# Optimization experiments

Measured on AMD Instinct MI355X. Metric: run time of the kernel, lower is better.

Reference implementation:

```python
import jax, jax.numpy as jnp
import numpy as np

B, G, T, N = 4, 8, 30, 60
CT, CN = 1, 60
FD, IDD = 256, 256
E = FD + IDD          # 512
H = 8                 # (FD+IDD)//head_dim
L = 6                 # num_layers
VP1 = 51              # num_id_vocabulary + 1
PE = 32               # rel_pe_length
DFF = 4 * E


def _ln(x, g, b, eps=1e-5):
    m = x.mean(-1, keepdims=True)
    v = ((x - m) ** 2).mean(-1, keepdims=True)
    return (x - m) / jnp.sqrt(v + eps) * g + b


def _mha(qx, kx, vx, Wqkv, bqkv, Wo, bo, bias, h):
    # torch nn.MultiheadAttention with add_zero_attn=True; bias is additive
    # attn bias of shape [B, h, Lq, Lk+1] (already padded for the zero-attn col).
    e = qx.shape[-1]
    d = e // h
    Wq, Wk, Wv = jnp.split(Wqkv, 3, axis=0)
    bq, bk, bv = jnp.split(bqkv, 3)
    q = qx @ Wq.T + bq
    k = kx @ Wk.T + bk
    v = vx @ Wv.T + bv
    b_, lq, _ = q.shape
    lk = k.shape[1]
    z = jnp.zeros((b_, 1, e), q.dtype)
    k = jnp.concatenate([k, z], axis=1)   # add_zero_attn appends zero key
    v = jnp.concatenate([v, z], axis=1)
    qh = q.reshape(b_, lq, h, d).transpose(0, 2, 1, 3)
    kh = k.reshape(b_, lk + 1, h, d).transpose(0, 2, 1, 3)
    vh = v.reshape(b_, lk + 1, h, d).transpose(0, 2, 1, 3)
    s = jnp.einsum('bhqd,bhkd->bhqk', qh, kh) / jnp.sqrt(jnp.float32(d)) + bias
    p = jax.nn.softmax(s, axis=-1)
    o = jnp.einsum('bhqk,bhkd->bhqd', p, vh).transpose(0, 2, 1, 3).reshape(b_, lq, e)
    return o @ Wo.T + bo


def _forward(tf, uf, ids, tt_, ut_, tm, um, Ww, Wout, rpe,
             saW, sab, saO, saob, sag, sabn,
             caW, cab, caO, caob, cag, cabn,
             f1, fb1, f2, fb2, fg, fbn):
    b, g, t, n, fd = tf.shape
    _, _, ct, cn, _ = uf.shape
    id_dim = Ww.shape[0]
    e = fd + id_dim
    nl = caW.shape[0]
    h = rpe.shape[-1]
    pe = rpe.shape[1]
    # one_hot(label) @ W_word.T == W_word[:, label]
    traj_id = Ww.T[ids]                                        # b g t n id
    unk_id = jnp.broadcast_to(Ww[:, VP1 - 1], (b, g, ct, cn, id_dim))
    traj = jnp.concatenate([tf, traj_id], -1).reshape(b * g, t * n, e)
    unk = jnp.concatenate([uf, unk_id], -1)                    # b g ct cn e

    tt = tt_.reshape(b * g, t * n)
    ut = ut_.reshape(b * g, ct * cn)
    neg = jnp.float32(-jnp.inf)
    zero = jnp.float32(0)
    causal = jnp.where(tt[:, None, :] >= ut[:, :, None], neg, zero)  # bg q k
    kpm = jnp.where(tm.reshape(b * g, t * n), neg, zero)             # bg k
    # torch rel_pos_map[u, t] = u - t; negative torch indices wrap -> mod pe
    rel_idx = (ut[:, :, None] - tt[:, None, :]) % pe                 # bg q k
    sa_bias = jnp.pad(
        jnp.where(um.reshape(b * g * ct, cn), neg, zero)[:, None, None, :],
        ((0, 0), (0, 0), (0, 0), (0, 1)))

    for l in range(nl):
        if l > 0:
            x = unk.reshape(b * g * ct, cn, e)
            y = _mha(x, x, x, saW[l - 1], sab[l - 1], saO[l - 1], saob[l - 1], sa_bias, h)
            unk = _ln(x + y, sag[l - 1], sabn[l - 1]).reshape(b, g, ct, cn, e)
        q = unk.reshape(b * g, ct * cn, e)
        rel = rpe[l][rel_idx]                                  # bg q k h  (gathered rel-PE)
        bias = causal[:, None] + jnp.transpose(rel, (0, 3, 1, 2)) + kpm[:, None, None, :]
        bias = jnp.pad(bias, ((0, 0), (0, 0), (0, 0), (0, 1)))
        y = _mha(q, traj, traj, caW[l], cab[l], caO[l], caob[l], bias, h)
        x = _ln(q + y, cag[l], cabn[l])
        hh = jax.nn.gelu(x @ f1[l].T + fb1[l], approximate=False) @ f2[l].T + fb2[l]
        x = _ln(x + hh, fg[l], fbn[l])
        unk = x.reshape(b, g, ct, cn, e)
    # final layer logits (eval mode): shared embed_to_word head, no bias
    return unk[..., fd:] @ Wout.T


def setup_inputs():
    key = jax.random.key(0)
    ks = iter(jax.random.split(key, 48))
    nrm = lambda shape, s=0.02: jax.random.normal(next(ks), shape, jnp.float32) * s
    return {
        'trajectory_features': jax.random.normal(next(ks), (B, G, T, N, FD), jnp.float32),
        'unknown_features': jax.random.normal(next(ks), (B, G, CT, CN, FD), jnp.float32),
        'trajectory_id_labels': jax.random.randint(next(ks), (B, G, T, N), 0, VP1),
        'trajectory_times': jax.random.randint(next(ks), (B, G, T, N), 0, PE),
        'unknown_times': jax.random.randint(next(ks), (B, G, CT, CN), 0, PE),
        'trajectory_masks': jnp.zeros((B, G, T, N), bool),
        'unknown_masks': jnp.zeros((B, G, CT, CN), bool),
        'use_decoder_checkpoint': 0,
        'W_word': nrm((IDD, VP1), 0.05),
        'W_out': nrm((VP1, IDD), 0.05),
        'rel_pos_embeds': nrm((L, PE, H), 0.1),
        'sa_Wqkv': nrm((L - 1, 3 * E, E)), 'sa_bqkv': jnp.zeros((L - 1, 3 * E)),
        'sa_Wo': nrm((L - 1, E, E)), 'sa_bo': jnp.zeros((L - 1, E)),
        'sa_ln_g': jnp.ones((L - 1, E)), 'sa_ln_b': jnp.zeros((L - 1, E)),
        'ca_Wqkv': nrm((L, 3 * E, E)), 'ca_bqkv': jnp.zeros((L, 3 * E)),
        'ca_Wo': nrm((L, E, E)), 'ca_bo': jnp.zeros((L, E)),
        'ca_ln_g': jnp.ones((L, E)), 'ca_ln_b': jnp.zeros((L, E)),
        'ffn_W1': nrm((L, DFF, E)), 'ffn_b1': jnp.zeros((L, DFF)),
        'ffn_W2': nrm((L, E, DFF)), 'ffn_b2': jnp.zeros((L, E)),
        'ffn_ln_g': jnp.ones((L, E)), 'ffn_ln_b': jnp.zeros((L, E)),
    }


def reference(trajectory_features, unknown_features, trajectory_id_labels,
              trajectory_times, unknown_times, trajectory_masks, unknown_masks,
              use_decoder_checkpoint, W_word, W_out, rel_pos_embeds,
              sa_Wqkv, sa_bqkv, sa_Wo, sa_bo, sa_ln_g, sa_ln_b,
              ca_Wqkv, ca_bqkv, ca_Wo, ca_bo, ca_ln_g, ca_ln_b,
              ffn_W1, ffn_b1, ffn_W2, ffn_b2, ffn_ln_g, ffn_ln_b):
    return _forward(trajectory_features, unknown_features, trajectory_id_labels,
                    trajectory_times, unknown_times, trajectory_masks, unknown_masks,
                    W_word, W_out, rel_pos_embeds,
                    sa_Wqkv, sa_bqkv, sa_Wo, sa_bo, sa_ln_g, sa_ln_b,
                    ca_Wqkv, ca_bqkv, ca_Wo, ca_bo, ca_ln_g, ca_ln_b,
                    ffn_W1, ffn_b1, ffn_W2, ffn_b2, ffn_ln_g, ffn_ln_b)
```

## Files before the change

kernel.cpp:

```cpp
#include <hip/hip_runtime.h>
#include <cmath>

__device__ __forceinline__ float bflo(unsigned int u) {
  union { unsigned int i; float f; } v; v.i = u << 16; return v.f;
}
__device__ __forceinline__ float bfhi(unsigned int u) {
  union { unsigned int i; float f; } v; v.i = u & 0xffff0000u; return v.f;
}
__device__ __forceinline__ float bf2f(unsigned short u) {
  union { unsigned int i; float f; } v; v.i = ((unsigned int)u) << 16; return v.f;
}
__device__ __forceinline__ unsigned short f2bf(float f) {
  union { float f; unsigned int i; } v; v.f = f;
  unsigned int i = v.i;
  return (unsigned short)((i + 0x7fffu + ((i >> 16) & 1u)) >> 16);
}

typedef __attribute__((ext_vector_type(8))) short short8;
typedef __attribute__((ext_vector_type(4))) float floatx4;

__global__ __launch_bounds__(256) void conv_kernel(
    const float* __restrict__ in, unsigned short* __restrict__ out, int n)
{
  int i = (blockIdx.x * 256 + threadIdx.x) << 2;
  if (i >= n) return;
  float4 v = *reinterpret_cast<const float4*>(in + i);
  ushort4 o;
  o.x = f2bf(v.x); o.y = f2bf(v.y); o.z = f2bf(v.z); o.w = f2bf(v.w);
  *reinterpret_cast<ushort4*>(out + i) = o;
}

__global__ __launch_bounds__(256) void gemm_mfma(
    const unsigned short* __restrict__ A, int lda,
    const unsigned short* __restrict__ W, int ldw,
    const float* __restrict__ bias,
    void* __restrict__ Cv, int ldc,
    int K, int act, int cbf16, int swz)
{
  __shared__ __align__(16) unsigned short As[2][128 * 32];
  __shared__ __align__(16) unsigned short Bs[2][128 * 32];
  const int tid = threadIdx.x;
  const int wave = tid >> 6, lane = tid & 63;

  int bxi = blockIdx.x, byi = blockIdx.y;
  if (swz) {
    int f = byi * gridDim.x + bxi;
    int q = (gridDim.x * gridDim.y) >> 3;
    f = (f & 7) * q + (f >> 3);
    bxi = f % gridDim.x;
    byi = f / gridDim.x;
  }
  const int bm = byi * 128, bn = bxi * 128;
  const int wm = (wave >> 1) << 6, wn = (wave & 1) << 6;

  floatx4 acc[4][4];
#pragma unroll
  for (int i = 0; i < 4; ++i)
#pragma unroll
    for (int j = 0; j < 4; ++j) acc[i][j] = (floatx4){0.f, 0.f, 0.f, 0.f};

  const int srow = (wave << 5) + (lane >> 2);
  const int chsw = (lane & 3) ^ ((srow >> 1) & 3);
  const int scol = chsw << 3;
  const unsigned short* Ag  = A + (size_t)(bm + srow) * lda + scol;
  const unsigned short* Wg  = W + (size_t)(bn + srow) * ldw + scol;
  const unsigned short* Ag2 = Ag + (size_t)16 * lda;
  const unsigned short* Wg2 = Wg + (size_t)16 * ldw;
  const int ldsw = (wave << 5) * 32;

  const int arow = lane & 15;
  const int rsw  = (arow >> 1) & 3;
  const int chrd = (lane >> 4) ^ rsw;
  const int aoff = (wm + arow) * 32 + (chrd << 3);
  const int boff = (wn + arow) * 32 + (chrd << 3);

  const int nt = K >> 5;

#define STAGE(b, t)                                                                 \
  do {                                                                              \
    const int k0_ = (t) << 5;                                                       \
    __builtin_amdgcn_global_load_lds(                                               \
        (const __attribute__((address_space(1))) unsigned int*)(Ag + k0_),          \
        (__attribute__((address_space(3))) unsigned int*)(As[(b)] + ldsw), 16, 0, 0); \
    __builtin_amdgcn_global_load_lds(                                               \
        (const __attribute__((address_space(1))) unsigned int*)(Ag2 + k0_),         \
        (__attribute__((address_space(3))) unsigned int*)(As[(b)] + ldsw + 16 * 32), 16, 0, 0); \
    __builtin_amdgcn_global_load_lds(                                               \
        (const __attribute__((address_space(1))) unsigned int*)(Wg + k0_),          \
        (__attribute__((address_space(3))) unsigned int*)(Bs[(b)] + ldsw), 16, 0, 0); \
    __builtin_amdgcn_global_load_lds(                                               \
        (const __attribute__((address_space(1))) unsigned int*)(Wg2 + k0_),         \
        (__attribute__((address_space(3))) unsigned int*)(Bs[(b)] + ldsw + 16 * 32), 16, 0, 0); \
  } while (0)

  STAGE(0, 0);
  if (nt > 1) STAGE(1, 1);

  int cur = 0;
  for (int t = 0; t < nt; ++t) {
    if (t + 1 < nt) asm volatile("s_waitcnt vmcnt(4)\n\ts_barrier" ::: "memory");
    else            asm volatile("s_waitcnt vmcnt(0)\n\ts_barrier" ::: "memory");

    short8 af[4], bf[4];
#pragma unroll
    for (int i = 0; i < 4; ++i) {
      af[i] = *reinterpret_cast<const short8*>(&As[cur][aoff + (i << 4) * 32]);
      bf[i] = *reinterpret_cast<const short8*>(&Bs[cur][boff + (i << 4) * 32]);
    }
    asm volatile("s_waitcnt lgkmcnt(0)\n\ts_barrier" ::: "memory");
    if (t + 2 < nt) STAGE(cur, t + 2);

#pragma unroll
    for (int i = 0; i < 4; ++i)
#pragma unroll
      for (int j = 0; j < 4; ++j)
        acc[i][j] = __builtin_amdgcn_mfma_f32_16x16x32_bf16(af[i], bf[j], acc[i][j], 0, 0, 0);
    cur ^= 1;
  }
#undef STAGE

  const int col0 = lane & 15;
  const int row0 = (lane >> 4) << 2;
#pragma unroll
  for (int i = 0; i < 4; ++i) {
#pragma unroll
    for (int j = 0; j < 4; ++j) {
      int col = bn + wn + (j << 4) + col0;
      float bv = bias ? bias[col] : 0.f;
#pragma unroll
      for (int r = 0; r < 4; ++r) {
        int row = bm + wm + (i << 4) + row0 + r;
        float v = acc[i][j][r] + bv;
        if (act) v = 0.5f * v * (1.f + erff(v * 0.70710678f));
        if (cbf16) ((unsigned short*)Cv)[(size_t)row * ldc + col] = f2bf(v);
        else       ((float*)Cv)[(size_t)row * ldc + col] = v;
      }
    }
  }
}

__device__ __forceinline__ float wred_max(float v) {
#pragma unroll
  for (int off = 32; off > 0; off >>= 1) v = fmaxf(v, __shfl_xor(v, off, 64));
  return v;
}
__device__ __forceinline__ float wred_sum(float v) {
#pragma unroll
  for (int off = 32; off > 0; off >>= 1) v += __shfl_xor(v, off, 64);
  return v;
}

#define LDK 72
__global__ __launch_bounds__(512) void attn_mfma_kernel(
    const unsigned short* __restrict__ Qp,
    const unsigned short* __restrict__ KVb,
    unsigned short* __restrict__ O,
    const int* __restrict__ tt, const int* __restrict__ ut,
    const unsigned char* __restrict__ km,
    const float* __restrict__ rel)
{
  const int bg = blockIdx.x >> 3, h = blockIdx.x & 7;
  const int tid = threadIdx.x;
  const int grp = tid >> 8;
  const int wave = (tid >> 6) & 3;
  const int lane = tid & 63;
  const int quad = lane >> 4, mrow = lane & 15;

  __shared__ __align__(16) unsigned short SMEM[6 * 64 * LDK];
  unsigned short* Ks = SMEM + grp * (3 * 64 * LDK);
  unsigned short* Vt = Ks + 64 * LDK;
  unsigned short* Ps = Vt + 64 * LDK;

  const int qa = wave * 16 + mrow;
  const int qc = qa < 60 ? qa : 59;
  const unsigned short* qptr = Qp + (size_t)(bg * 60 + qc) * 512 + h * 64 + quad * 8;
  const short8 af0 = *reinterpret_cast<const short8*>(qptr);
  const short8 af1 = *reinterpret_cast<const short8*>(qptr + 32);

  const float relreg = rel[(lane & 31) * 8 + h];

  int tq[4];
  float m[4], l[4];
  floatx4 acc[4];
#pragma unroll
  for (int r = 0; r < 4; ++r) {
    int qo = wave * 16 + quad * 4 + r;
    tq[r] = ut[bg * 60 + (qo < 60 ? qo : 59)];
    m[r] = grp ? -1e30f : 0.f;
    l[r] = grp ? 0.f : 1.f;
  }
#pragma unroll
  for (int nt = 0; nt < 4; ++nt) acc[nt] = (floatx4){0.f, 0.f, 0.f, 0.f};

  const int sk = tid & 255;
  const int stok = sk >> 2, schk = sk & 3;

  for (int it = 0; it < 15; ++it) {
    const int k0 = (grp + 2 * it) << 6;
    __syncthreads();
    {
      const int key = k0 + stok;
      uint4 kr0 = {0,0,0,0}, kr1 = {0,0,0,0}, vr0 = {0,0,0,0}, vr1 = {0,0,0,0};
      if (key < 1800) {
        const unsigned short* kb = KVb + ((size_t)bg * 1800 + key) * 1024 + h * 64 + schk * 16;
        kr0 = *reinterpret_cast<const uint4*>(kb);
        kr1 = *reinterpret_cast<const uint4*>(kb + 8);
        vr0 = *reinterpret_cast<const uint4*>(kb + 512);
        vr1 = *reinterpret_cast<const uint4*>(kb + 520);
      }
      *reinterpret_cast<uint4*>(&Ks[stok * LDK + schk * 16]) = kr0;
      *reinterpret_cast<uint4*>(&Ks[stok * LDK + schk * 16 + 8]) = kr1;
      unsigned int wv[8] = {vr0.x, vr0.y, vr0.z, vr0.w, vr1.x, vr1.y, vr1.z, vr1.w};
#pragma unroll
      for (int e = 0; e < 16; ++e)
        Vt[(schk * 16 + e) * LDK + stok] = (unsigned short)(wv[e >> 1] >> ((e & 1) * 16));
    }
    int meta = 0x10000;
    {
      int kk = k0 + lane;
      if (kk < 1800) {
        int base = bg * 1800 + kk;
        meta = tt[base] | (km[base] ? 0x10000 : 0);
      }
    }
    __syncthreads();

    floatx4 S[4];
#pragma unroll
    for (int nt = 0; nt < 4; ++nt) {
      const unsigned short* kb = Ks + (nt * 16 + mrow) * LDK + quad * 8;
      short8 b0 = *reinterpret_cast<const short8*>(kb);
      short8 b1 = *reinterpret_cast<const short8*>(kb + 32);
      floatx4 s = (floatx4){0.f, 0.f, 0.f, 0.f};
      s = __builtin_amdgcn_mfma_f32_16x16x32_bf16(af0, b0, s, 0, 0, 0);
      s = __builtin_amdgcn_mfma_f32_16x16x32_bf16(af1, b1, s, 0, 0, 0);
      S[nt] = s;
    }
    int mcol[4];
#pragma unroll
    for (int nt = 0; nt < 4; ++nt)
      mcol[nt] = __builtin_amdgcn_ds_bpermute((nt * 16 + mrow) << 2, meta);
    float sv[4][4];
#pragma unroll
    for (int nt = 0; nt < 4; ++nt) {
      int tk = mcol[nt] & 0xffff;
      int bad0 = mcol[nt] >> 16;
#pragma unroll
      for (int r = 0; r < 4; ++r) {
        float v = S[nt][r] * 0.125f;
        int ridx = (tq[r] - tk) & 31;
        v += __int_as_float(__builtin_amdgcn_ds_bpermute(ridx << 2, __float_as_int(relreg)));
        sv[nt][r] = (bad0 | (tk >= tq[r])) ? -1e30f : v;
      }
    }
#pragma unroll
    for (int r = 0; r < 4; ++r) {
      float rm = fmaxf(fmaxf(sv[0][r], sv[1][r]), fmaxf(sv[2][r], sv[3][r]));
#pragma unroll
      for (int d = 1; d < 16; d <<= 1) rm = fmaxf(rm, __shfl_xor(rm, d, 64));
      float nm = fmaxf(m[r], rm);
      float corr = __expf(m[r] - nm);
      float ps = 0.f;
      const int prow = (wave * 16 + quad * 4 + r) * LDK + mrow;
#pragma unroll
      for (int nt = 0; nt < 4; ++nt) {
        float p = __expf(sv[nt][r] - nm);
        ps += p;
        Ps[prow + nt * 16] = f2bf(p);
      }
#pragma unroll
      for (int d = 1; d < 16; d <<= 1) ps += __shfl_xor(ps, d, 64);
      l[r] = l[r] * corr + ps;
      m[r] = nm;
#pragma unroll
      for (int nt = 0; nt < 4; ++nt) acc[nt][r] *= corr;
    }
    const unsigned short* pp = Ps + (wave * 16 + mrow) * LDK + quad * 8;
    short8 a0 = *reinterpret_cast<const short8*>(pp);
    short8 a1 = *reinterpret_cast<const short8*>(pp + 32);
#pragma unroll
    for (int nt = 0; nt < 4; ++nt) {
      const unsigned short* vb = Vt + (nt * 16 + mrow) * LDK + quad * 8;
      short8 b0 = *reinterpret_cast<const short8*>(vb);
      short8 b1 = *reinterpret_cast<const short8*>(vb + 32);
      acc[nt] = __builtin_amdgcn_mfma_f32_16x16x32_bf16(a0, b0, acc[nt], 0, 0, 0);
      acc[nt] = __builtin_amdgcn_mfma_f32_16x16x32_bf16(a1, b1, acc[nt], 0, 0, 0);
    }
  }

  __syncthreads();
  float* MA = (float*)SMEM;
  float* Ml = (float*)(SMEM + 64 * 68 * 2);
  float* Ll = Ml + 64;
  if (grp == 1) {
#pragma unroll
    for (int r = 0; r < 4; ++r) {
      int row = wave * 16 + quad * 4 + r;
#pragma unroll
      for (int nt = 0; nt < 4; ++nt)
        MA[row * 68 + nt * 16 + mrow] = acc[nt][r];
      if (mrow == 0) { Ml[row] = m[r]; Ll[row] = l[r]; }
    }
  }
  __syncthreads();
  if (grp == 0) {
#pragma unroll
    for (int r = 0; r < 4; ++r) {
      int row = wave * 16 + quad * 4 + r;
      float m1 = Ml[row], l1 = Ll[row];
      float M = fmaxf(m[r], m1);
      float c0 = __expf(m[r] - M), c1 = __expf(m1 - M);
      float invL = 1.f / (l[r] * c0 + l1 * c1);
      if (row < 60) {
        unsigned short* op = O + (size_t)(bg * 60 + row) * 512 + h * 64;
#pragma unroll
        for (int nt = 0; nt < 4; ++nt) {
          float o = (acc[nt][r] * c0 + MA[row * 68 + nt * 16 + mrow] * c1) * invL;
          op[nt * 16 + mrow] = f2bf(o);
        }
      }
    }
  }
}

#define QPB 32
#define QPW 8
__global__ __launch_bounds__(256) void attn2_kernel(
    const unsigned short* __restrict__ Qp, int qs,
    const unsigned short* __restrict__ Kp, int ks,
    const unsigned short* __restrict__ Vp, int vs,
    unsigned short* __restrict__ O, int os, int kLen,
    const unsigned char* __restrict__ kmask)
{
  const int bg = blockIdx.x >> 3;
  const int h  = blockIdx.x & 7;
  const int q0 = blockIdx.y * QPB;
  const int tid = threadIdx.x;
  const int wave = tid >> 6, lane = tid & 63;

  __shared__ float Qs[QPB][68];
  __shared__ float Ks[64][68];
  __shared__ float Vs[64][68];
  __shared__ float Ps[QPB][68];

  {
    int qr = tid >> 3, j = tid & 7;
    int q = q0 + qr;
    float f[8] = {0, 0, 0, 0, 0, 0, 0, 0};
    if (q < 60) {
      uint4 v = *reinterpret_cast<const uint4*>(Qp + (size_t)(bg * 60 + q) * qs + h * 64 + j * 8);
      f[0] = bflo(v.x); f[1] = bfhi(v.x); f[2] = bflo(v.y); f[3] = bfhi(v.y);
      f[4] = bflo(v.z); f[5] = bfhi(v.z); f[6] = bflo(v.w); f[7] = bfhi(v.w);
    }
#pragma unroll
    for (int e = 0; e < 8; ++e) Qs[qr][j * 8 + e] = f[e];
  }

  float m[QPW], l[QPW], acc[QPW];
#pragma unroll
  for (int i = 0; i < QPW; ++i) { m[i] = 0.f; l[i] = 1.f; acc[i] = 0.f; }

  const int std = tid >> 2;
  const int stj = tid & 3;

  for (int k0 = 0; k0 < kLen; k0 += 64) {
    __syncthreads();
    const bool sok = (k0 + std) < kLen;
    {
      const unsigned short* kb = Kp + ((size_t)bg * kLen + k0 + std) * ks + h * 64 + stj * 16;
      float f[16];
#pragma unroll
      for (int e = 0; e < 16; ++e) f[e] = 0.f;
      if (sok) {
        uint4 v0 = *reinterpret_cast<const uint4*>(kb);
        uint4 v1 = *reinterpret_cast<const uint4*>(kb + 8);
        f[0] = bflo(v0.x); f[1] = bfhi(v0.x); f[2]  = bflo(v0.y); f[3]  = bfhi(v0.y);
        f[4] = bflo(v0.z); f[5] = bfhi(v0.z); f[6]  = bflo(v0.w); f[7]  = bfhi(v0.w);
        f[8] = bflo(v1.x); f[9] = bfhi(v1.x); f[10] = bflo(v1.y); f[11] = bfhi(v1.y);
        f[12] = bflo(v1.z); f[13] = bfhi(v1.z); f[14] = bflo(v1.w); f[15] = bfhi(v1.w);
      }
#pragma unroll
      for (int e = 0; e < 16; ++e) Ks[stj * 16 + e][std] = f[e];
    }
    {
      const unsigned short* vb = Vp + ((size_t)bg * kLen + k0 + std) * vs + h * 64;
#pragma unroll
      for (int c = 0; c < 2; ++c) {
        int off = c * 32 + stj * 8;
        float f[8] = {0, 0, 0, 0, 0, 0, 0, 0};
        if (sok) {
          uint4 v = *reinterpret_cast<const uint4*>(vb + off);
          f[0] = bflo(v.x); f[1] = bfhi(v.x); f[2] = bflo(v.y); f[3] = bfhi(v.y);
          f[4] = bflo(v.z); f[5] = bfhi(v.z); f[6] = bflo(v.w); f[7] = bfhi(v.w);
        }
#pragma unroll
        for (int e = 0; e < 8; ++e) Vs[std][off + e] = f[e];
      }
    }
    const int kk = k0 + lane;
    const bool kok = kk < kLen;
    unsigned char kmv = 0;
    if (kok && kmask) kmv = kmask[(size_t)bg * kLen + kk];
    __syncthreads();

    float s[QPW];
#pragma unroll
    for (int i = 0; i < QPW; ++i) s[i] = 0.f;
    for (int d = 0; d < 64; ++d) {
      float kv = Ks[d][lane];
#pragma unroll
      for (int i = 0; i < QPW; ++i)
        s[i] = fmaf(Qs[wave * QPW + i][d], kv, s[i]);
    }

    const int kmax = min(64, kLen - k0);
#pragma unroll
    for (int i = 0; i < QPW; ++i) {
      float svv = s[i] * 0.125f;
      if (kmv || !kok) svv = -1e30f;
      float nm = fmaxf(m[i], wred_max(svv));
      float p = __expf(svv - nm);
      float ts = wred_sum(p);
      float corr = __expf(m[i] - nm);
      l[i] = l[i] * corr + ts;
      acc[i] *= corr;
      m[i] = nm;
      Ps[wave * QPW + i][lane] = p;
    }
    for (int k = 0; k < kmax; ++k) {
      float v = Vs[k][lane];
#pragma unroll
      for (int i = 0; i < QPW; ++i)
        acc[i] = fmaf(Ps[wave * QPW + i][k], v, acc[i]);
    }
  }

#pragma unroll
  for (int i = 0; i < QPW; ++i) {
    int q = q0 + wave * QPW + i;
    if (q < 60)
      O[(size_t)(bg * 60 + q) * os + h * 64 + lane] = f2bf(acc[i] / l[i]);
  }
}

__global__ __launch_bounds__(256) void add_ln_kernel(
    const float* __restrict__ a, const float* __restrict__ b,
    const float* __restrict__ g, const float* __restrict__ be,
    float* __restrict__ o, unsigned short* __restrict__ ob)
{
  const int t = blockIdx.x;
  const int tid = threadIdx.x;
  const int wave = tid >> 6, lane = tid & 63;
  const size_t base = (size_t)t * 512;
  float v0 = a[base + tid] + b[base + tid];
  float v1 = a[base + 256 + tid] + b[base + 256 + tid];
  __shared__ float red[4];
  float s = wred_sum(v0 + v1);
  if (lane == 0) red[wave] = s;
  __syncthreads();
  float mean = (red[0] + red[1] + red[2] + red[3]) * (1.0f / 512.0f);
  float d0 = v0 - mean, d1 = v1 - mean;
  float vs = wred_sum(d0 * d0 + d1 * d1);
  __syncthreads();
  if (lane == 0) red[wave] = vs;
  __syncthreads();
  float var = (red[0] + red[1] + red[2] + red[3]) * (1.0f / 512.0f);
  float rstd = rsqrtf(var + 1e-5f);
  float r0 = d0 * rstd * g[tid] + be[tid];
  float r1 = d1 * rstd * g[256 + tid] + be[256 + tid];
  o[base + tid] = r0;
  o[base + 256 + tid] = r1;
  ob[base + tid] = f2bf(r0);
  ob[base + 256 + tid] = f2bf(r1);
}

__global__ __launch_bounds__(256) void build_traj_kernel(
    const float* __restrict__ tf, const int* __restrict__ ids,
    const float* __restrict__ Ww, unsigned short* __restrict__ traj)
{
  int idx = blockIdx.x * 256 + threadIdx.x;
  int tok = idx >> 9;
  int j = idx & 511;
  float v = (j < 256) ? tf[((size_t)tok << 8) + j] : Ww[(j - 256) * 51 + ids[tok]];
  traj[idx] = f2bf(v);
}

__global__ __launch_bounds__(256) void build_unk_kernel(
    const float* __restrict__ uf, const float* __restrict__ Ww,
    float* __restrict__ x, unsigned short* __restrict__ xb)
{
  int idx = blockIdx.x * 256 + threadIdx.x;
  int tok = idx >> 9;
  int j = idx & 511;
  float v = (j < 256) ? uf[((size_t)tok << 8) + j] : Ww[(j - 256) * 51 + 50];
  x[idx] = v;
  xb[idx] = f2bf(v);
}

__global__ __launch_bounds__(64) void head_kernel(
    const float* __restrict__ x, const float* __restrict__ Wout, float* __restrict__ out)
{
  const int t = blockIdx.x;
  const int tid = threadIdx.x;
  __shared__ float xs[256];
  for (int i = tid; i < 256; i += 64) xs[i] = x[(size_t)t * 512 + 256 + i];
  __syncthreads();
  if (tid < 51) {
    const float* w = Wout + tid * 256;
    float s = 0.f;
    for (int k = 0; k < 256; ++k) s = fmaf(xs[k], w[k], s);
    out[t * 51 + tid] = s;
  }
}

extern "C" void kernel_launch(void* const* d_in, const int* in_sizes, int n_in,
                              void* d_out, int out_size, void* d_ws, size_t ws_size,
                              hipStream_t stream) {
  const float* tf  = (const float*)d_in[0];
  const float* uf  = (const float*)d_in[1];
  const int*   ids = (const int*)d_in[2];
  const int*   tt  = (const int*)d_in[3];
  const int*   ut  = (const int*)d_in[4];
  const unsigned char* tm = (const unsigned char*)d_in[5];
  const unsigned char* um = (const unsigned char*)d_in[6];
  const float* Ww   = (const float*)d_in[8];
  const float* Wout = (const float*)d_in[9];
  const float* rpe  = (const float*)d_in[10];
  const float* saW  = (const float*)d_in[11];
  const float* sab  = (const float*)d_in[12];
  const float* saO  = (const float*)d_in[13];
  const float* saob = (const float*)d_in[14];
  const float* sag  = (const float*)d_in[15];
  const float* sabn = (const float*)d_in[16];
  const float* caW  = (const float*)d_in[17];
  const float* cab  = (const float*)d_in[18];
  const float* caO  = (const float*)d_in[19];
  const float* caob = (const float*)d_in[20];
  const float* cag  = (const float*)d_in[21];
  const float* cabn = (const float*)d_in[22];
  const float* f1   = (const float*)d_in[23];
  const float* fb1  = (const float*)d_in[24];
  const float* f2   = (const float*)d_in[25];
  const float* fb2  = (const float*)d_in[26];
  const float* fg   = (const float*)d_in[27];
  const float* fbn  = (const float*)d_in[28];

  unsigned short* trajb = (unsigned short*)d_ws;
  unsigned short* KVb   = trajb + (size_t)29491200;
  unsigned short* qkvb  = KVb   + (size_t)58982400;
  unsigned short* hb    = qkvb  + (size_t)2949120;
  unsigned short* xb    = hb    + (size_t)3932160;
  float* x    = (float*)(xb + (size_t)983040);
  float* ybuf = x + (size_t)983040;
  unsigned short* wtail = (unsigned short*)(ybuf + (size_t)983040);

  const size_t NEED = (size_t)200540160 + (size_t)24117248 * 2;
  const bool pre = ws_size >= NEED;
  unsigned short* wsa  = wtail;
  unsigned short* wsaO = wsa  + (size_t)3932160;
  unsigned short* wca  = wsaO + (size_t)1310720;
  unsigned short* wcaO = wca  + (size_t)4718592;
  unsigned short* wf1  = wcaO + (size_t)1572864;
  unsigned short* wf2  = wf1  + (size_t)6291456;
  unsigned short* wconv = wtail;

  if (pre) {
    conv_kernel<<<dim3(3840), dim3(256), 0, stream>>>(saW, wsa, 3932160);
    conv_kernel<<<dim3(1280), dim3(256), 0, stream>>>(saO, wsaO, 1310720);
    conv_kernel<<<dim3(4608), dim3(256), 0, stream>>>(caW, wca, 4718592);
    conv_kernel<<<dim3(1536), dim3(256), 0, stream>>>(caO, wcaO, 1572864);
    conv_kernel<<<dim3(6144), dim3(256), 0, stream>>>(f1, wf1, 6291456);
    conv_kernel<<<dim3(6144), dim3(256), 0, stream>>>(f2, wf2, 6291456);
  }

  build_traj_kernel<<<dim3(115200), dim3(256), 0, stream>>>(tf, ids, Ww, trajb);
  build_unk_kernel<<<dim3(3840), dim3(256), 0, stream>>>(uf, Ww, x, xb);

  for (int l = 0; l < 6; ++l) {
    if (l > 0) {
      int sl = l - 1;
      const unsigned short* wq;
      if (pre) wq = wsa + (size_t)sl * 786432;
      else {
        conv_kernel<<<dim3(768), dim3(256), 0, stream>>>(saW + (size_t)sl * 786432, wconv, 786432);
        wq = wconv;
      }
      gemm_mfma<<<dim3(12, 15), dim3(256), 0, stream>>>(
          xb, 512, wq, 512, sab + sl * 1536, qkvb, 1536, 512, 0, 1, 0);
      attn2_kernel<<<dim3(256, 2), dim3(256), 0, stream>>>(
          qkvb, 1536, qkvb + 512, 1536, qkvb + 1024, 1536, hb, 512, 60, um);
      const unsigned short* wo;
      if (pre) wo = wsaO + (size_t)sl * 262144;
      else {
        conv_kernel<<<dim3(256), dim3(256), 0, stream>>>(saO + (size_t)sl * 262144, wconv, 262144);
        wo = wconv;
      }
      gemm_mfma<<<dim3(4, 15), dim3(256), 0, stream>>>(
          hb, 512, wo, 512, saob + sl * 512, ybuf, 512, 512, 0, 0, 0);
      add_ln_kernel<<<dim3(1920), dim3(256), 0, stream>>>(x, ybuf, sag + sl * 512, sabn + sl * 512, x, xb);
    }
    const unsigned short* wqkv;
    if (pre) wqkv = wca + (size_t)l * 786432;
    else {
      conv_kernel<<<dim3(768), dim3(256), 0, stream>>>(caW + (size_t)l * 786432, wconv, 786432);
      wqkv = wconv;
    }
    gemm_mfma<<<dim3(8, 450), dim3(256), 0, stream>>>(
        trajb, 512, wqkv + 262144, 512, cab + l * 1536 + 512, KVb, 1024, 512, 0, 1, 1);
    gemm_mfma<<<dim3(4, 15), dim3(256), 0, stream>>>(
        xb, 512, wqkv, 512, cab + l * 1536, qkvb, 512, 512, 0, 1, 0);
    attn_mfma_kernel<<<dim3(256), dim3(512), 0, stream>>>(
        qkvb, KVb, hb, tt, ut, tm, rpe + l * 256);
    const unsigned short* wco;
    if (pre) wco = wcaO + (size_t)l * 262144;
    else {
      conv_kernel<<<dim3(256), dim3(256), 0, stream>>>(caO + (size_t)l * 262144, wconv, 262144);
      wco = wconv;
    }
    gemm_mfma<<<dim3(4, 15), dim3(256), 0, stream>>>(
        hb, 512, wco, 512, caob + l * 512, ybuf, 512, 512, 0, 0, 0);
    add_ln_kernel<<<dim3(1920), dim3(256), 0, stream>>>(x, ybuf, cag + l * 512, cabn + l * 512, x, xb);
    const unsigned short* w1;
    if (pre) w1 = wf1 + (size_t)l * 1048576;
    else {
      conv_kernel<<<dim3(1024), dim3(256), 0, stream>>>(f1 + (size_t)l * 1048576, wconv, 1048576);
      w1 = wconv;
    }
    gemm_mfma<<<dim3(16, 15), dim3(256), 0, stream>>>(
        xb, 512, w1, 512, fb1 + l * 2048, hb, 2048, 512, 1, 1, 0);
    const unsigned short* w2;
    if (pre) w2 = wf2 + (size_t)l * 1048576;
    else {
      conv_kernel<<<dim3(1024), dim3(256), 0, stream>>>(f2 + (size_t)l * 1048576, wconv, 1048576);
      w2 = wconv;
    }
    gemm_mfma<<<dim3(4, 15), dim3(256), 0, stream>>>(
        hb, 2048, w2, 2048, fb2 + l * 512, ybuf, 512, 2048, 0, 0, 0);
    add_ln_kernel<<<dim3(1920), dim3(256), 0, stream>>>(x, ybuf, fg + l * 512, fbn + l * 512, x, xb);
  }
  head_kernel<<<dim3(1920), dim3(64), 0, stream>>>(x, Wout, (float*)d_out);
}
```

Measured before the change: 1.995 ms.

## Add 256x256-tile GEMM with direct-to-LDS loads for cross-attention KV projection

Adds a dedicated 256x256 tile GEMM kernel for the large cross-attention K/V projection (57600x1024x512). It uses 512 threads, double-buffered LDS filled by global_load_lds, swizzled LDS reads, fine-grained staging interleaved with MFMA blocks, s_setprio and an XCD-aware block remap. The aim is more operand reuse per tile and better overlap of loads with compute than the generic 128x128 gemm_mfma. In exchange it hardcodes K=512, N=1024 and M divisible by 256, and its large register footprint may limit occupancy.

```diff
diff --git a/kernel.cpp b/kernel.cpp
--- a/kernel.cpp
+++ b/kernel.cpp
@@ -28,6 +28,165 @@
   ushort4 o;
   o.x = f2bf(v.x); o.y = f2bf(v.y); o.z = f2bf(v.z); o.w = f2bf(v.w);
   *reinterpret_cast<ushort4*>(out + i) = o;
+}
+
+__global__ __launch_bounds__(512, 2) void gemm256(
+    const unsigned short* __restrict__ A,
+    const unsigned short* __restrict__ W,
+    const float* __restrict__ bias,
+    unsigned short* __restrict__ C)
+{
+  __shared__ __align__(16) unsigned short LA[2][2][8192];
+  __shared__ __align__(16) unsigned short LB[2][2][8192];
+  const int tid = threadIdx.x;
+  const int wave = tid >> 6, lane = tid & 63;
+  const int quad = lane >> 4, mrow = lane & 15;
+  const int wm = wave >> 2, wn = wave & 3;
+  const size_t ldK = 512;
+  const int nt = 8;
+
+  int f = blockIdx.x;
+  {
+    const int nwg = gridDim.x;
+    const int q = nwg >> 3, r = nwg & 7;
+    const int x = f & 7, i = f >> 3;
+    f = (x < r ? x * (q + 1) : r * (q + 1) + (x - r) * q) + i;
+  }
+  const int bn = (f & 3) << 8;
+  const int bm = (f >> 2) << 8;
+
+  floatx4 acc[8][4];
+#pragma unroll
+  for (int i = 0; i < 8; ++i)
+#pragma unroll
+    for (int j = 0; j < 4; ++j) acc[i][j] = (floatx4){0.f, 0.f, 0.f, 0.f};
+
+  const int srow0 = (wave << 4) + (lane >> 2);
+  const int srow1 = srow0 + 128;
+  const int sslot = (lane & 3) ^ (srow0 & 3);
+
+#define STAGEH(dst, srcbase, rowoff, kelem)                                          \
+  do {                                                                               \
+    __builtin_amdgcn_global_load_lds(                                                \
+        (const __attribute__((address_space(1))) unsigned int*)(                     \
+            (srcbase) + (size_t)((rowoff) + srow0) * ldK + (kelem) + sslot * 8),     \
+        (__attribute__((address_space(3))) unsigned int*)((dst) + wave * 512),       \
+        16, 0, 0);                                                                   \
+    __builtin_amdgcn_global_load_lds(                                                \
+        (const __attribute__((address_space(1))) unsigned int*)(                     \
+            (srcbase) + (size_t)((rowoff) + srow1) * ldK + (kelem) + sslot * 8),     \
+        (__attribute__((address_space(3))) unsigned int*)((dst) + 4096 + wave * 512),\
+        16, 0, 0);                                                                   \
+  } while (0)
+
+  STAGEH(&LB[0][0][0], W, bn, 0);
+  STAGEH(&LA[0][0][0], A, bm, 0);
+  STAGEH(&LB[0][1][0], W, bn, 32);
+  STAGEH(&LA[0][1][0], A, bm, 32);
+  STAGEH(&LB[1][0][0], W, bn, 64);
+  STAGEH(&LA[1][0][0], A, bm, 64);
+  STAGEH(&LB[1][1][0], W, bn, 96);
+  asm volatile("s_waitcnt vmcnt(6)" ::: "memory");
+  __builtin_amdgcn_s_barrier();
+
+  const int rsw = ((quad ^ (mrow & 3)) << 3);
+  const int arowb = wm * 128 + mrow;
+  const int brows = wn * 64 + mrow;
+
+  for (int T = 0; T < nt; ++T) {
+    const int c = T & 1;
+    unsigned short* A0 = &LA[c][0][0];
+    unsigned short* A1 = &LA[c][1][0];
+    unsigned short* B0 = &LB[c][0][0];
+    unsigned short* B1 = &LB[c][1][0];
+    short8 afr[4], bfr[4];
+
+#pragma unroll
+    for (int i = 0; i < 4; ++i)
+      afr[i] = *reinterpret_cast<const short8*>(A0 + (arowb + i * 16) * 32 + rsw);
+#pragma unroll
+    for (int j = 0; j < 4; ++j)
+      bfr[j] = *reinterpret_cast<const short8*>(B0 + (brows + j * 16) * 32 + rsw);
+    if (T + 1 < nt) STAGEH(&LA[c ^ 1][1][0], A, bm, (T + 1) * 64 + 32);
+    __builtin_amdgcn_s_barrier();
+    asm volatile("s_waitcnt lgkmcnt(0)" ::: "memory");
+    __builtin_amdgcn_s_setprio(1);
+#pragma unroll
+    for (int i = 0; i < 4; ++i)
+#pragma unroll
+      for (int j = 0; j < 4; ++j)
+        acc[i][j] = __builtin_amdgcn_mfma_f32_16x16x32_bf16(afr[i], bfr[j], acc[i][j], 0, 0, 0);
+    __builtin_amdgcn_s_setprio(0);
+    __builtin_amdgcn_s_barrier();
+
+#pragma unroll
+    for (int i = 0; i < 4; ++i)
+      afr[i] = *reinterpret_cast<const short8*>(A0 + (arowb + (i + 4) * 16) * 32 + rsw);
+    if (T + 2 < nt) STAGEH(&LB[c][0][0], W, bn, (T + 2) * 64);
+    __builtin_amdgcn_s_barrier();
+    asm volatile("s_waitcnt lgkmcnt(0)" ::: "memory");
+    __builtin_amdgcn_s_setprio(1);
+#pragma unroll
+    for (int i = 0; i < 4; ++i)
+#pragma unroll
+      for (int j = 0; j < 4; ++j)
+        acc[i + 4][j] = __builtin_amdgcn_mfma_f32_16x16x32_bf16(afr[i], bfr[j], acc[i + 4][j], 0, 0, 0);
+    __builtin_amdgcn_s_setprio(0);
+    __builtin_amdgcn_s_barrier();
+
+#pragma unroll
+    for (int i = 0; i < 4; ++i)
+      afr[i] = *reinterpret_cast<const short8*>(A1 + (arowb + i * 16) * 32 + rsw);
+#pragma unroll
+    for (int j = 0; j < 4; ++j)
+      bfr[j] = *reinterpret_cast<const short8*>(B1 + (brows + j * 16) * 32 + rsw);
+    if (T + 2 < nt) STAGEH(&LA[c][0][0], A, bm, (T + 2) * 64);
+    __builtin_amdgcn_s_barrier();
+    asm volatile("s_waitcnt lgkmcnt(0)" ::: "memory");
+    __builtin_amdgcn_s_setprio(1);
+#pragma unroll
+    for (int i = 0; i < 4; ++i)
+#pragma unroll
+      for (int j = 0; j < 4; ++j)
+        acc[i][j] = __builtin_amdgcn_mfma_f32_16x16x32_bf16(afr[i], bfr[j], acc[i][j], 0, 0, 0);
+    __builtin_amdgcn_s_setprio(0);
+    __builtin_amdgcn_s_barrier();
+
+#pragma unroll
+    for (int i = 0; i < 4; ++i)
+      afr[i] = *reinterpret_cast<const short8*>(A1 + (arowb + (i + 4) * 16) * 32 + rsw);
+    if (T + 2 < nt) STAGEH(&LB[c][1][0], W, bn, (T + 2) * 64 + 32);
+    __builtin_amdgcn_s_barrier();
+    asm volatile("s_waitcnt lgkmcnt(0)" ::: "memory");
+    __builtin_amdgcn_s_setprio(1);
+#pragma unroll
+    for (int i = 0; i < 4; ++i)
+#pragma unroll
+      for (int j = 0; j < 4; ++j)
+        acc[i + 4][j] = __builtin_amdgcn_mfma_f32_16x16x32_bf16(afr[i], bfr[j], acc[i + 4][j], 0, 0, 0);
+    __builtin_amdgcn_s_setprio(0);
+    if (T + 2 < nt)
+      asm volatile("s_waitcnt vmcnt(6)" ::: "memory");
+    else
+      asm volatile("s_waitcnt vmcnt(0)" ::: "memory");
+    __builtin_amdgcn_s_barrier();
+  }
+#undef STAGEH
+
+  const int col0 = lane & 15;
+  const int row0 = (lane >> 4) << 2;
+#pragma unroll
+  for (int i = 0; i < 8; ++i)
+#pragma unroll
+    for (int j = 0; j < 4; ++j) {
+      int col = bn + wn * 64 + j * 16 + col0;
+      float bv = bias[col];
+#pragma unroll
+      for (int r = 0; r < 4; ++r) {
+        int row = bm + wm * 128 + i * 16 + row0 + r;
+        C[(size_t)row * 1024 + col] = f2bf(acc[i][j][r] + bv);
+      }
+    }
 }
 
 __global__ __launch_bounds__(256) void gemm_mfma(
@@ -605,8 +764,8 @@
       conv_kernel<<<dim3(768), dim3(256), 0, stream>>>(caW + (size_t)l * 786432, wconv, 786432);
       wqkv = wconv;
     }
-    gemm_mfma<<<dim3(8, 450), dim3(256), 0, stream>>>(
-        trajb, 512, wqkv + 262144, 512, cab + l * 1536 + 512, KVb, 1024, 512, 0, 1, 1);
+    gemm256<<<dim3(900), dim3(512), 0, stream>>>(
+        trajb, wqkv + 262144, cab + l * 1536 + 512, KVb);
     gemm_mfma<<<dim3(4, 15), dim3(256), 0, stream>>>(
         xb, 512, wqkv, 512, cab + l * 1536, qkvb, 512, 512, 0, 1, 0);
     attn_mfma_kernel<<<dim3(256), dim3(512), 0, stream>>>(
```

Result: faster. 1.945 ms (-2.5%).
